# Kernel tuning notes

Hardware: AMD Instinct MI355X
Metric: run time of the kernel (lower is better)

Reference implementation:

```python
import jax, jax.numpy as jnp
import numpy as np

V, J, NB = 6890, 52, 16
NPOSE = (J - 1) * 9  # 459 pose-blendshape features
# Standard SMPL-H kinematic tree: 22 body joints + left hand (wrist 20) + right hand (wrist 21)
PARENTS = np.array([
    -1, 0, 0, 0, 1, 2, 3, 4, 5, 6, 7, 8, 9, 9, 9, 12, 13, 14, 16, 17, 18, 19,
    20, 22, 23, 20, 25, 26, 20, 28, 29, 20, 31, 32, 20, 34, 35,
    21, 37, 38, 21, 40, 41, 21, 43, 44, 21, 46, 47, 21, 49, 50
], dtype=np.int32)


def rot6d_to_matrix(d6):
    # d6: (..., 6) -> (..., 3, 3), rows are the Gram-Schmidt basis (pytorch3d convention)
    a1, a2 = d6[..., :3], d6[..., 3:]
    b1 = a1 / jnp.linalg.norm(a1, axis=-1, keepdims=True)
    a2p = a2 - jnp.sum(b1 * a2, axis=-1, keepdims=True) * b1
    b2 = a2p / jnp.linalg.norm(a2p, axis=-1, keepdims=True)
    b3 = jnp.cross(b1, b2)
    return jnp.stack([b1, b2, b3], axis=-2)


def rigid_transform(rot_mats, joints):
    # rot_mats: (B, J, 3, 3); joints: (B, J, 3) -> relative transforms (B, J, 4, 4)
    rel = jnp.concatenate(
        [joints[..., :1, :], joints[..., 1:, :] - joints[..., PARENTS[1:], :]], axis=-2)
    tm = jnp.concatenate([rot_mats, rel[..., None]], axis=-1)  # (B, J, 3, 4)
    bottom = jnp.zeros(tm.shape[:-2] + (1, 4), dtype=tm.dtype).at[..., 0, 3].set(1.0)
    tm = jnp.concatenate([tm, bottom], axis=-2)  # (B, J, 4, 4)
    chain = [tm[..., 0, :, :]]
    for i in range(1, J):  # fixed 52-joint tree, unrolled
        chain.append(chain[int(PARENTS[i])] @ tm[..., i, :, :])
    transforms = jnp.stack(chain, axis=-3)  # (B, J, 4, 4)
    t_corr = jnp.einsum('bjcd,bjd->bjc', transforms[..., :3, :3], joints)
    return transforms.at[..., :3, 3].add(-t_corr)


def lbs_forward(body_pose, betas, global_orient, transl,
                v_template, shapedirs, posedirs, J_template, J_shapedirs, lbs_weights):
    full_pose = jnp.concatenate([global_orient, body_pose], axis=-2)  # (B, 52, 6)
    rot_mats = rot6d_to_matrix(full_pose)                              # (B, 52, 3, 3)
    joints = J_template + jnp.einsum('bk,jck->bjc', betas, J_shapedirs)
    A = rigid_transform(rot_mats, joints)                              # (B, 52, 4, 4)
    eye = jnp.eye(3, dtype=rot_mats.dtype)
    pose_feature = (rot_mats[..., 1:, :, :] - eye).reshape(rot_mats.shape[0], NPOSE)
    v_posed = (v_template
               + jnp.einsum('bk,vck->bvc', betas, shapedirs)
               + jnp.einsum('bk,kvc->bvc', pose_feature, posedirs))    # (B, V, 3)
    T = jnp.einsum('vj,bjcd->bvcd', lbs_weights, A)                    # (B, V, 4, 4)
    verts = jnp.einsum('bvcd,bvd->bvc', T[..., :3, :3], v_posed) + T[..., :3, 3]
    return verts + transl[..., None, :]


def setup_inputs() -> dict:
    key = jax.random.key(0)
    ks = jax.random.split(key, 10)
    B = 1024
    return {
        'body_pose': jax.random.normal(ks[0], (B, J - 1, 6), jnp.float32),
        'betas': jax.random.normal(ks[1], (B, NB), jnp.float32),
        'global_orient': jax.random.normal(ks[2], (B, 1, 6), jnp.float32),
        'transl': jax.random.normal(ks[3], (B, 3), jnp.float32),
        'v_template': jax.random.normal(ks[4], (V, 3), jnp.float32) * 0.3,
        'shapedirs': jax.random.normal(ks[5], (V, 3, NB), jnp.float32) * 0.01,
        'posedirs': jax.random.normal(ks[6], (NPOSE, V, 3), jnp.float32) * 0.01,
        'J_template': jax.random.normal(ks[7], (J, 3), jnp.float32) * 0.3,
        'J_shapedirs': jax.random.normal(ks[8], (J, 3, NB), jnp.float32) * 0.01,
        'lbs_weights': jax.nn.softmax(jax.random.normal(ks[9], (V, J), jnp.float32) * 2.0, axis=-1),
    }


def reference(body_pose, betas, global_orient, transl,
              v_template, shapedirs, posedirs, J_template, J_shapedirs, lbs_weights):
    return lbs_forward(body_pose, betas, global_orient, transl,
                       v_template, shapedirs, posedirs, J_template, J_shapedirs, lbs_weights)
```

## Files before the change

kernel.cpp:

```cpp
#include <hip/hip_runtime.h>

typedef unsigned short u16;
typedef __bf16  bf16x8 __attribute__((ext_vector_type(8)));
typedef float   f32x4  __attribute__((ext_vector_type(4)));
typedef unsigned int u32x4 __attribute__((ext_vector_type(4)));

#define B_SZ   1024
#define V_SZ   6890
#define VPADB  6912
#define J_SZ   52
#define NB_SZ  16
#define NPOSE  459
#define N3     20670
#define NPAD   20736
#define KG     480
#define KA     160
#define MROWS  12288

__constant__ int PARENTS_D[52] = {-1,0,0,0,1,2,3,4,5,6,7,8,9,9,9,12,13,14,16,17,18,19,20,22,23,
                                  20,25,26,20,28,29,20,31,32,20,34,35,21,37,38,21,40,41,21,43,44,
                                  21,46,47,21,49,50};

__device__ __forceinline__ u16 f2b(float f) {
  union { float f; unsigned u; } v; v.f = f;
  unsigned r = (v.u + 0x7FFFu + ((v.u >> 16) & 1u)) >> 16;
  return (u16)r;
}
__device__ __forceinline__ float b2f(u16 h) {
  union { unsigned u; float f; } v; v.u = ((unsigned)h) << 16;
  return v.f;
}
__device__ __forceinline__ void async16(const void* g, void* l) {
  __builtin_amdgcn_global_load_lds((const __attribute__((address_space(1))) void*)g,
                                   (__attribute__((address_space(3))) void*)l, 16, 0, 0);
}

__global__ __launch_bounds__(256) void k0_build_pdt(const float* __restrict__ posedirs,
                                                    const float* __restrict__ shapedirs,
                                                    u16* __restrict__ PDt)
{
  __shared__ u16 tile[32][33];
  const int tx = threadIdx.x;
  const int ty = threadIdx.y;
  const int n0 = blockIdx.x * 32;
  const int k0 = blockIdx.y * 32;
#pragma unroll
  for (int i = 0; i < 4; ++i) {
    int k = k0 + ty + i*8;
    int n = n0 + tx;
    float val = 0.f;
    if (n < N3) {
      if (k < NPOSE)              val = posedirs[(size_t)k * N3 + n];
      else if (k < NPOSE + NB_SZ) val = shapedirs[(size_t)n * NB_SZ + (k - NPOSE)];
    }
    tile[ty + i*8][tx] = f2b(val);
  }
  __syncthreads();
#pragma unroll
  for (int i = 0; i < 4; ++i) {
    int n = n0 + ty + i*8;
    int k = k0 + tx;
    PDt[(size_t)n * KG + k] = tile[tx][ty + i*8];
  }
}

__global__ __launch_bounds__(256) void k0w_build_wb(const float* __restrict__ lbsw,
                                                    u16* __restrict__ WB)
{
  __shared__ __align__(16) u16 wtile[64 * KA];
  const int tid = threadIdx.x;
  const int v0  = blockIdx.x * 64;
  const int vl  = tid >> 2;
  const int v   = v0 + vl;
  const int jseg = (tid & 3) * 13;

  wtile[(tid >> 2) * KA + 156 + (tid & 3)] = 0;

#pragma unroll
  for (int jj = 0; jj < 13; ++jj) {
    int j = jseg + jj;
    float wv = (v < V_SZ) ? lbsw[(size_t)v * J_SZ + j] : 0.f;
    u16 hi = f2b(wv);
    u16 lo = f2b(wv - b2f(hi));
    wtile[vl * KA + j]        = hi;
    wtile[vl * KA + 52 + j]   = hi;
    wtile[vl * KA + 104 + j]  = lo;
  }
  __syncthreads();
  u32x4*       dst = (u32x4*)(WB + (size_t)v0 * KA);
  const u32x4* src = (const u32x4*)wtile;
  for (int i = tid; i < 64 * KA / 8; i += 256) dst[i] = src[i];
}

__global__ __launch_bounds__(64) void k1_prep(const float* __restrict__ body_pose,
                                              const float* __restrict__ betas,
                                              const float* __restrict__ global_orient,
                                              const float* __restrict__ J_template,
                                              const float* __restrict__ J_shapedirs,
                                              u16* __restrict__ AH,
                                              u16* __restrict__ PF)
{
  __shared__ float R[J_SZ][9];
  __shared__ float jts[J_SZ][3];
  __shared__ float G[J_SZ][12];
  __shared__ u16   AHs[12 * KA];
  const int b   = blockIdx.x;
  const int tid = threadIdx.x;

  for (int i = tid; i < 12 * KA / 2; i += 64) ((unsigned*)AHs)[i] = 0u;

  if (tid < J_SZ) {
    const float* d6 = (tid == 0) ? &global_orient[(size_t)b * 6]
                                 : &body_pose[((size_t)b * 51 + (tid - 1)) * 6];
    float a1x = d6[0], a1y = d6[1], a1z = d6[2];
    float a2x = d6[3], a2y = d6[4], a2z = d6[5];
    float inv1 = rsqrtf(a1x*a1x + a1y*a1y + a1z*a1z);
    float b1x = a1x*inv1, b1y = a1y*inv1, b1z = a1z*inv1;
    float d   = b1x*a2x + b1y*a2y + b1z*a2z;
    float ux = a2x - d*b1x, uy = a2y - d*b1y, uz = a2z - d*b1z;
    float inv2 = rsqrtf(ux*ux + uy*uy + uz*uz);
    float b2x = ux*inv2, b2y = uy*inv2, b2z = uz*inv2;
    float b3x = b1y*b2z - b1z*b2y;
    float b3y = b1z*b2x - b1x*b2z;
    float b3z = b1x*b2y - b1y*b2x;
    R[tid][0]=b1x; R[tid][1]=b1y; R[tid][2]=b1z;
    R[tid][3]=b2x; R[tid][4]=b2y; R[tid][5]=b2z;
    R[tid][6]=b3x; R[tid][7]=b3y; R[tid][8]=b3z;
#pragma unroll
    for (int c = 0; c < 3; ++c) {
      float s = J_template[tid*3 + c];
#pragma unroll
      for (int k = 0; k < NB_SZ; ++k)
        s += betas[(size_t)b*NB_SZ + k] * J_shapedirs[(tid*3 + c)*NB_SZ + k];
      jts[tid][c] = s;
    }
  }
  __syncthreads();

  if (tid == 0) {
#pragma unroll
    for (int c = 0; c < 3; ++c) {
      G[0][c*4+0] = R[0][c*3+0];
      G[0][c*4+1] = R[0][c*3+1];
      G[0][c*4+2] = R[0][c*3+2];
      G[0][c*4+3] = jts[0][c];
    }
    for (int j = 1; j < J_SZ; ++j) {
      int p = PARENTS_D[j];
      float r0 = jts[j][0] - jts[p][0];
      float r1 = jts[j][1] - jts[p][1];
      float r2 = jts[j][2] - jts[p][2];
      for (int c = 0; c < 3; ++c) {
        float g0 = G[p][c*4+0], g1 = G[p][c*4+1], g2 = G[p][c*4+2];
        G[j][c*4+0] = g0*R[j][0] + g1*R[j][3] + g2*R[j][6];
        G[j][c*4+1] = g0*R[j][1] + g1*R[j][4] + g2*R[j][7];
        G[j][c*4+2] = g0*R[j][2] + g1*R[j][5] + g2*R[j][8];
        G[j][c*4+3] = g0*r0 + g1*r1 + g2*r2 + G[p][c*4+3];
      }
    }
  }
  __syncthreads();

  if (tid < J_SZ) {
    float o[12];
#pragma unroll
    for (int i = 0; i < 12; ++i) o[i] = G[tid][i];
#pragma unroll
    for (int c = 0; c < 3; ++c)
      o[c*4+3] -= o[c*4+0]*jts[tid][0] + o[c*4+1]*jts[tid][1] + o[c*4+2]*jts[tid][2];
#pragma unroll
    for (int cd = 0; cd < 12; ++cd) {
      u16 hi = f2b(o[cd]);
      u16 lo = f2b(o[cd] - b2f(hi));
      AHs[cd*KA + tid]        = hi;
      AHs[cd*KA + 52 + tid]   = lo;
      AHs[cd*KA + 104 + tid]  = hi;
    }
  }

  for (int k = tid; k < KG; k += 64) {
    float val = 0.f;
    if (k < NPOSE) {
      int j  = k / 9 + 1;
      int rc = k - (j - 1) * 9;
      val = R[j][rc] - ((rc == 0 || rc == 4 || rc == 8) ? 1.f : 0.f);
    } else if (k < NPOSE + NB_SZ) {
      val = betas[(size_t)b*NB_SZ + (k - NPOSE)];
    }
    PF[(size_t)b*KG + k] = f2b(val);
  }

  __syncthreads();
  unsigned* dst = (unsigned*)(AH + (size_t)b * 12 * KA);
  for (int i = tid; i < 12 * KA / 2; i += 64) dst[i] = ((const unsigned*)AHs)[i];
}

__global__ __launch_bounds__(256) void k2_gemm(const u16* __restrict__ PF,
                                               const u16* __restrict__ PDt,
                                               const float* __restrict__ vtmpl,
                                               u16* __restrict__ VP)
{
  __shared__ __align__(16) u16 lA[128*32];
  __shared__ __align__(16) u16 lB[128*32];
  const int tid  = threadIdx.x;
  const int lane = tid & 63;
  const int w    = tid >> 6;
  const int n0   = blockIdx.x * 128;
  const int b0   = blockIdx.y * 128;
  const int moff = (w & 1) * 64;
  const int noff = (w >> 1) * 64;
  const int q    = lane >> 4;
  const int lrow = lane & 15;

  f32x4 acc[4][4];
#pragma unroll
  for (int i = 0; i < 4; ++i)
#pragma unroll
    for (int j = 0; j < 4; ++j) { f32x4 z = {0.f,0.f,0.f,0.f}; acc[i][j] = z; }

  int aoff[4], boff[4];
#pragma unroll
  for (int i = 0; i < 4; ++i) {
    int ra = moff + i*16 + lrow;
    aoff[i] = ra*32 + (q ^ ((ra + (ra >> 2)) & 3)) * 8;
    int rb = noff + i*16 + lrow;
    boff[i] = rb*32 + (q ^ ((rb + (rb >> 2)) & 3)) * 8;
  }
  int srow[2], schunk[2];
#pragma unroll
  for (int t = 0; t < 2; ++t) {
    int i = (t*4 + w)*64 + lane;
    int r = i >> 2;
    srow[t]   = r;
    schunk[t] = (i & 3) ^ ((r + (r >> 2)) & 3);
  }

  for (int k0 = 0; k0 < KG; k0 += 32) {
#pragma unroll
    for (int t = 0; t < 2; ++t) {
      async16(PF  + (size_t)(b0 + srow[t])*KG + k0 + schunk[t]*8, &lA[(t*4 + w)*512]);
      async16(PDt + (size_t)(n0 + srow[t])*KG + k0 + schunk[t]*8, &lB[(t*4 + w)*512]);
    }
    __syncthreads();
    bf16x8 af[4], bfv[4];
#pragma unroll
    for (int i = 0; i < 4; ++i) af[i]  = *(const bf16x8*)&lA[aoff[i]];
#pragma unroll
    for (int i = 0; i < 4; ++i) bfv[i] = *(const bf16x8*)&lB[boff[i]];
#pragma unroll
    for (int i = 0; i < 4; ++i)
#pragma unroll
      for (int j = 0; j < 4; ++j)
        acc[i][j] = __builtin_amdgcn_mfma_f32_16x16x32_bf16(af[i], bfv[j], acc[i][j], 0, 0, 0);
    __syncthreads();
  }

#pragma unroll
  for (int i = 0; i < 4; ++i) {
    int brow = b0 + moff + i*16 + q*4;
#pragma unroll
    for (int j = 0; j < 4; ++j) {
      int n = n0 + noff + j*16 + lrow;
      if (n < N3) {
        float bias = vtmpl[n];
#pragma unroll
        for (int r = 0; r < 4; ++r)
          VP[(size_t)(brow + r)*NPAD + n] = f2b(acc[i][j][r] + bias);
      }
    }
  }
}

__global__ __launch_bounds__(256) void k4_blend(const u16* __restrict__ AH,
                                                const u16* __restrict__ WB,
                                                const u16* __restrict__ VP,
                                                const float* __restrict__ transl,
                                                float* __restrict__ out)
{
  __shared__ __align__(16) u16 lA[2][4096];
  __shared__ __align__(16) u16 lB[2][4096];
  const int tid  = threadIdx.x;
  const int lane = tid & 63;
  const int w    = tid >> 6;
  const int n0   = blockIdx.x * 128;
  const int m0   = blockIdx.y * 128;
  const int moff = (w & 1) * 64;
  const int noff = (w >> 1) * 64;
  const int q    = lane >> 4;
  const int lrow = lane & 15;

  int srow[2], schunk[2];
#pragma unroll
  for (int t = 0; t < 2; ++t) {
    int i = (t*4 + w)*64 + lane;
    int r = i >> 2;
    srow[t]   = r;
    schunk[t] = (i & 3) ^ ((r + (r >> 2)) & 3);
  }

#define K4_STAGE(buf, seg)                                                          \
  {                                                                                 \
    const int kk = (seg) * 32;                                                      \
    _Pragma("unroll")                                                               \
    for (int t = 0; t < 2; ++t) {                                                   \
      async16(AH + (size_t)(m0 + srow[t])*KA + kk + schunk[t]*8,                    \
              &lA[buf][(t*4 + w)*512]);                                             \
      async16(WB + (size_t)(n0 + srow[t])*KA + kk + schunk[t]*8,                    \
              &lB[buf][(t*4 + w)*512]);                                             \
    }                                                                               \
  }

  K4_STAGE(0, 0);

  int   bp[4], cp[4];
  float tr[4];
#pragma unroll
  for (int i = 0; i < 4; ++i) {
    int gq = (m0 + moff + i*16) / 4 + q;
    bp[i] = gq / 3;
    cp[i] = gq - bp[i]*3;
    tr[i] = transl[bp[i]*3 + cp[i]];
  }
  u16 pv[4][4][3];
#pragma unroll
  for (int i = 0; i < 4; ++i) {
    const u16* vpb = VP + (size_t)bp[i] * NPAD;
#pragma unroll
    for (int j = 0; j < 4; ++j) {
      const int v = n0 + noff + j*16 + lrow;
      pv[i][j][0] = vpb[(size_t)v*3 + 0];
      pv[i][j][1] = vpb[(size_t)v*3 + 1];
      pv[i][j][2] = vpb[(size_t)v*3 + 2];
    }
  }

  f32x4 acc[4][4];
#pragma unroll
  for (int i = 0; i < 4; ++i)
#pragma unroll
    for (int j = 0; j < 4; ++j) { f32x4 z = {0.f,0.f,0.f,0.f}; acc[i][j] = z; }

  int aoff[4], boff[4];
#pragma unroll
  for (int i = 0; i < 4; ++i) {
    int ra = moff + i*16 + lrow;
    aoff[i] = ra*32 + (q ^ ((ra + (ra >> 2)) & 3)) * 8;
    int rb = noff + i*16 + lrow;
    boff[i] = rb*32 + (q ^ ((rb + (rb >> 2)) & 3)) * 8;
  }

  __syncthreads();

#pragma unroll
  for (int seg = 0; seg < 5; ++seg) {
    const int cur = seg & 1;
    if (seg < 4) K4_STAGE(cur ^ 1, seg + 1);
    bf16x8 af[4], bfv[4];
#pragma unroll
    for (int i = 0; i < 4; ++i) af[i]  = *(const bf16x8*)&lA[cur][aoff[i]];
#pragma unroll
    for (int i = 0; i < 4; ++i) bfv[i] = *(const bf16x8*)&lB[cur][boff[i]];
#pragma unroll
    for (int i = 0; i < 4; ++i)
#pragma unroll
      for (int j = 0; j < 4; ++j)
        acc[i][j] = __builtin_amdgcn_mfma_f32_16x16x32_bf16(af[i], bfv[j], acc[i][j], 0, 0, 0);
    if (seg < 4) __syncthreads();
  }
#undef K4_STAGE

#pragma unroll
  for (int i = 0; i < 4; ++i) {
    float* ob = out + (size_t)bp[i] * (V_SZ * 3);
#pragma unroll
    for (int j = 0; j < 4; ++j) {
      const int v = n0 + noff + j*16 + lrow;
      if (v < V_SZ) {
        float p0 = b2f(pv[i][j][0]);
        float p1 = b2f(pv[i][j][1]);
        float p2 = b2f(pv[i][j][2]);
        f32x4 a = acc[i][j];
        ob[(size_t)v*3 + cp[i]] = a[0]*p0 + a[1]*p1 + a[2]*p2 + a[3] + tr[i];
      }
    }
  }
}

extern "C" void kernel_launch(void* const* d_in, const int* in_sizes, int n_in,
                              void* d_out, int out_size, void* d_ws, size_t ws_size,
                              hipStream_t stream) {
  const float* body_pose     = (const float*)d_in[0];
  const float* betas         = (const float*)d_in[1];
  const float* global_orient = (const float*)d_in[2];
  const float* transl        = (const float*)d_in[3];
  const float* v_template    = (const float*)d_in[4];
  const float* shapedirs     = (const float*)d_in[5];
  const float* posedirs      = (const float*)d_in[6];
  const float* J_template    = (const float*)d_in[7];
  const float* J_shapedirs   = (const float*)d_in[8];
  const float* lbsw          = (const float*)d_in[9];
  float* out = (float*)d_out;

  char* ws = (char*)d_ws;
  u16* PF  = (u16*)(ws);
  u16* AH  = (u16*)(ws + 1048576u);
  u16* WB  = (u16*)(ws + 6291456u);
  u16* PDt = (u16*)(ws + 8503296u);
  u16* VP  = (u16*)(ws + 28409856u);

  k0_build_pdt<<<dim3(648, 15), dim3(32, 8), 0, stream>>>(posedirs, shapedirs, PDt);
  k0w_build_wb<<<dim3(VPADB / 64), dim3(256), 0, stream>>>(lbsw, WB);
  k1_prep<<<dim3(1024), dim3(64), 0, stream>>>(body_pose, betas, global_orient,
                                               J_template, J_shapedirs, AH, PF);
  k2_gemm<<<dim3(162, 8), dim3(256), 0, stream>>>(PF, PDt, v_template, VP);
  k4_blend<<<dim3(VPADB / 128, MROWS / 128), dim3(256), 0, stream>>>(AH, WB, VP, transl, out);
}
```

Measured before the change: 280.2 us.

## Merge prep kernels into one launch and double-buffer GEMM LDS loads

Result: faster. 269.1 us (-4.0%).

```diff
diff --git a/kernel.cpp b/kernel.cpp
--- a/kernel.cpp
+++ b/kernel.cpp
@@ -17,6 +17,10 @@
 #define KA     160
 #define MROWS  12288
 
+#define NK1    (B_SZ / 4)
+#define NK0W   (VPADB / 64)
+#define NK0    (648 * 15)
+
 __constant__ int PARENTS_D[52] = {-1,0,0,0,1,2,3,4,5,6,7,8,9,9,9,12,13,14,16,17,18,19,20,22,23,
                                   20,25,26,20,28,29,20,31,32,20,34,35,21,37,38,21,40,41,21,43,44,
                                   21,46,47,21,49,50};
@@ -35,122 +39,74 @@
                                    (__attribute__((address_space(3))) void*)l, 16, 0, 0);
 }
 
-__global__ __launch_bounds__(256) void k0_build_pdt(const float* __restrict__ posedirs,
-                                                    const float* __restrict__ shapedirs,
-                                                    u16* __restrict__ PDt)
-{
-  __shared__ u16 tile[32][33];
-  const int tx = threadIdx.x;
-  const int ty = threadIdx.y;
-  const int n0 = blockIdx.x * 32;
-  const int k0 = blockIdx.y * 32;
-#pragma unroll
-  for (int i = 0; i < 4; ++i) {
-    int k = k0 + ty + i*8;
-    int n = n0 + tx;
-    float val = 0.f;
-    if (n < N3) {
-      if (k < NPOSE)              val = posedirs[(size_t)k * N3 + n];
-      else if (k < NPOSE + NB_SZ) val = shapedirs[(size_t)n * NB_SZ + (k - NPOSE)];
-    }
-    tile[ty + i*8][tx] = f2b(val);
-  }
-  __syncthreads();
-#pragma unroll
-  for (int i = 0; i < 4; ++i) {
-    int n = n0 + ty + i*8;
-    int k = k0 + tx;
-    PDt[(size_t)n * KG + k] = tile[tx][ty + i*8];
-  }
-}
-
-__global__ __launch_bounds__(256) void k0w_build_wb(const float* __restrict__ lbsw,
-                                                    u16* __restrict__ WB)
-{
-  __shared__ __align__(16) u16 wtile[64 * KA];
-  const int tid = threadIdx.x;
-  const int v0  = blockIdx.x * 64;
-  const int vl  = tid >> 2;
-  const int v   = v0 + vl;
-  const int jseg = (tid & 3) * 13;
-
-  wtile[(tid >> 2) * KA + 156 + (tid & 3)] = 0;
-
-#pragma unroll
-  for (int jj = 0; jj < 13; ++jj) {
-    int j = jseg + jj;
-    float wv = (v < V_SZ) ? lbsw[(size_t)v * J_SZ + j] : 0.f;
-    u16 hi = f2b(wv);
-    u16 lo = f2b(wv - b2f(hi));
-    wtile[vl * KA + j]        = hi;
-    wtile[vl * KA + 52 + j]   = hi;
-    wtile[vl * KA + 104 + j]  = lo;
-  }
-  __syncthreads();
-  u32x4*       dst = (u32x4*)(WB + (size_t)v0 * KA);
-  const u32x4* src = (const u32x4*)wtile;
-  for (int i = tid; i < 64 * KA / 8; i += 256) dst[i] = src[i];
-}
-
-__global__ __launch_bounds__(64) void k1_prep(const float* __restrict__ body_pose,
+__global__ __launch_bounds__(256) void k_prep(const float* __restrict__ posedirs,
+                                              const float* __restrict__ shapedirs,
+                                              const float* __restrict__ lbsw,
+                                              const float* __restrict__ body_pose,
                                               const float* __restrict__ betas,
                                               const float* __restrict__ global_orient,
                                               const float* __restrict__ J_template,
                                               const float* __restrict__ J_shapedirs,
+                                              u16* __restrict__ PDt,
+                                              u16* __restrict__ WB,
                                               u16* __restrict__ AH,
                                               u16* __restrict__ PF)
 {
-  __shared__ float R[J_SZ][9];
-  __shared__ float jts[J_SZ][3];
-  __shared__ float G[J_SZ][12];
-  __shared__ u16   AHs[12 * KA];
-  const int b   = blockIdx.x;
+  __shared__ __align__(16) char smem[35328];
+  const int bid = blockIdx.x;
   const int tid = threadIdx.x;
 
-  for (int i = tid; i < 12 * KA / 2; i += 64) ((unsigned*)AHs)[i] = 0u;
-
-  if (tid < J_SZ) {
-    const float* d6 = (tid == 0) ? &global_orient[(size_t)b * 6]
-                                 : &body_pose[((size_t)b * 51 + (tid - 1)) * 6];
-    float a1x = d6[0], a1y = d6[1], a1z = d6[2];
-    float a2x = d6[3], a2y = d6[4], a2z = d6[5];
-    float inv1 = rsqrtf(a1x*a1x + a1y*a1y + a1z*a1z);
-    float b1x = a1x*inv1, b1y = a1y*inv1, b1z = a1z*inv1;
-    float d   = b1x*a2x + b1y*a2y + b1z*a2z;
-    float ux = a2x - d*b1x, uy = a2y - d*b1y, uz = a2z - d*b1z;
-    float inv2 = rsqrtf(ux*ux + uy*uy + uz*uz);
-    float b2x = ux*inv2, b2y = uy*inv2, b2z = uz*inv2;
-    float b3x = b1y*b2z - b1z*b2y;
-    float b3y = b1z*b2x - b1x*b2z;
-    float b3z = b1x*b2y - b1y*b2x;
-    R[tid][0]=b1x; R[tid][1]=b1y; R[tid][2]=b1z;
-    R[tid][3]=b2x; R[tid][4]=b2y; R[tid][5]=b2z;
-    R[tid][6]=b3x; R[tid][7]=b3y; R[tid][8]=b3z;
-#pragma unroll
-    for (int c = 0; c < 3; ++c) {
-      float s = J_template[tid*3 + c];
-#pragma unroll
-      for (int k = 0; k < NB_SZ; ++k)
-        s += betas[(size_t)b*NB_SZ + k] * J_shapedirs[(tid*3 + c)*NB_SZ + k];
-      jts[tid][c] = s;
-    }
-  }
-  __syncthreads();
-
-  if (tid == 0) {
-#pragma unroll
-    for (int c = 0; c < 3; ++c) {
+  if (bid < NK1) {
+    const int g = tid >> 6;
+    const int t = tid & 63;
+    const int b = bid * 4 + g;
+    char* base = smem + g * 8832;
+    float (*R)[9]   = (float(*)[9])(base);
+    float (*jts)[3] = (float(*)[3])(base + 1872);
+    float (*G)[12]  = (float(*)[12])(base + 2496);
+    u16*   AHs      = (u16*)(base + 4992);
+
+    for (int i = t; i < 12 * KA / 2; i += 64) ((unsigned*)AHs)[i] = 0u;
+
+    if (t < J_SZ) {
+      const float* d6 = (t == 0) ? &global_orient[(size_t)b * 6]
+                                 : &body_pose[((size_t)b * 51 + (t - 1)) * 6];
+      float a1x = d6[0], a1y = d6[1], a1z = d6[2];
+      float a2x = d6[3], a2y = d6[4], a2z = d6[5];
+      float inv1 = rsqrtf(a1x*a1x + a1y*a1y + a1z*a1z);
+      float b1x = a1x*inv1, b1y = a1y*inv1, b1z = a1z*inv1;
+      float d   = b1x*a2x + b1y*a2y + b1z*a2z;
+      float ux = a2x - d*b1x, uy = a2y - d*b1y, uz = a2z - d*b1z;
+      float inv2 = rsqrtf(ux*ux + uy*uy + uz*uz);
+      float b2x = ux*inv2, b2y = uy*inv2, b2z = uz*inv2;
+      float b3x = b1y*b2z - b1z*b2y;
+      float b3y = b1z*b2x - b1x*b2z;
+      float b3z = b1x*b2y - b1y*b2x;
+      R[t][0]=b1x; R[t][1]=b1y; R[t][2]=b1z;
+      R[t][3]=b2x; R[t][4]=b2y; R[t][5]=b2z;
+      R[t][6]=b3x; R[t][7]=b3y; R[t][8]=b3z;
+#pragma unroll
+      for (int c = 0; c < 3; ++c) {
+        float s = J_template[t*3 + c];
+#pragma unroll
+        for (int k = 0; k < NB_SZ; ++k)
+          s += betas[(size_t)b*NB_SZ + k] * J_shapedirs[(t*3 + c)*NB_SZ + k];
+        jts[t][c] = s;
+      }
+    }
+    __syncthreads();
+
+    if (t < 3) {
+      const int c = t;
       G[0][c*4+0] = R[0][c*3+0];
       G[0][c*4+1] = R[0][c*3+1];
       G[0][c*4+2] = R[0][c*3+2];
       G[0][c*4+3] = jts[0][c];
-    }
-    for (int j = 1; j < J_SZ; ++j) {
-      int p = PARENTS_D[j];
-      float r0 = jts[j][0] - jts[p][0];
-      float r1 = jts[j][1] - jts[p][1];
-      float r2 = jts[j][2] - jts[p][2];
-      for (int c = 0; c < 3; ++c) {
+      for (int j = 1; j < J_SZ; ++j) {
+        int p = PARENTS_D[j];
+        float r0 = jts[j][0] - jts[p][0];
+        float r1 = jts[j][1] - jts[p][1];
+        float r2 = jts[j][2] - jts[p][2];
         float g0 = G[p][c*4+0], g1 = G[p][c*4+1], g2 = G[p][c*4+2];
         G[j][c*4+0] = g0*R[j][0] + g1*R[j][3] + g2*R[j][6];
         G[j][c*4+1] = g0*R[j][1] + g1*R[j][4] + g2*R[j][7];
@@ -158,41 +114,91 @@
         G[j][c*4+3] = g0*r0 + g1*r1 + g2*r2 + G[p][c*4+3];
       }
     }
-  }
-  __syncthreads();
-
-  if (tid < J_SZ) {
-    float o[12];
-#pragma unroll
-    for (int i = 0; i < 12; ++i) o[i] = G[tid][i];
-#pragma unroll
-    for (int c = 0; c < 3; ++c)
-      o[c*4+3] -= o[c*4+0]*jts[tid][0] + o[c*4+1]*jts[tid][1] + o[c*4+2]*jts[tid][2];
-#pragma unroll
-    for (int cd = 0; cd < 12; ++cd) {
-      u16 hi = f2b(o[cd]);
-      u16 lo = f2b(o[cd] - b2f(hi));
-      AHs[cd*KA + tid]        = hi;
-      AHs[cd*KA + 52 + tid]   = lo;
-      AHs[cd*KA + 104 + tid]  = hi;
-    }
-  }
-
-  for (int k = tid; k < KG; k += 64) {
-    float val = 0.f;
-    if (k < NPOSE) {
-      int j  = k / 9 + 1;
-      int rc = k - (j - 1) * 9;
-      val = R[j][rc] - ((rc == 0 || rc == 4 || rc == 8) ? 1.f : 0.f);
-    } else if (k < NPOSE + NB_SZ) {
-      val = betas[(size_t)b*NB_SZ + (k - NPOSE)];
-    }
-    PF[(size_t)b*KG + k] = f2b(val);
-  }
-
-  __syncthreads();
-  unsigned* dst = (unsigned*)(AH + (size_t)b * 12 * KA);
-  for (int i = tid; i < 12 * KA / 2; i += 64) dst[i] = ((const unsigned*)AHs)[i];
+    __syncthreads();
+
+    if (t < J_SZ) {
+      float o[12];
+#pragma unroll
+      for (int i = 0; i < 12; ++i) o[i] = G[t][i];
+#pragma unroll
+      for (int c = 0; c < 3; ++c)
+        o[c*4+3] -= o[c*4+0]*jts[t][0] + o[c*4+1]*jts[t][1] + o[c*4+2]*jts[t][2];
+#pragma unroll
+      for (int cd = 0; cd < 12; ++cd) {
+        u16 hi = f2b(o[cd]);
+        u16 lo = f2b(o[cd] - b2f(hi));
+        AHs[cd*KA + t]        = hi;
+        AHs[cd*KA + 52 + t]   = lo;
+        AHs[cd*KA + 104 + t]  = hi;
+      }
+    }
+
+    for (int k = t; k < KG; k += 64) {
+      float val = 0.f;
+      if (k < NPOSE) {
+        int j  = k / 9 + 1;
+        int rc = k - (j - 1) * 9;
+        val = R[j][rc] - ((rc == 0 || rc == 4 || rc == 8) ? 1.f : 0.f);
+      } else if (k < NPOSE + NB_SZ) {
+        val = betas[(size_t)b*NB_SZ + (k - NPOSE)];
+      }
+      PF[(size_t)b*KG + k] = f2b(val);
+    }
+
+    __syncthreads();
+    unsigned* dst = (unsigned*)(AH + (size_t)b * 12 * KA);
+    for (int i = t; i < 12 * KA / 2; i += 64) dst[i] = ((const unsigned*)AHs)[i];
+
+  } else if (bid < NK1 + NK0W) {
+    u16* wtile = (u16*)smem;
+    const int v0  = (bid - NK1) * 64;
+    const int vl  = tid >> 2;
+    const int v   = v0 + vl;
+    const int jseg = (tid & 3) * 13;
+
+    wtile[vl * KA + 156 + (tid & 3)] = 0;
+
+#pragma unroll
+    for (int jj = 0; jj < 13; ++jj) {
+      int j = jseg + jj;
+      float wv = (v < V_SZ) ? lbsw[(size_t)v * J_SZ + j] : 0.f;
+      u16 hi = f2b(wv);
+      u16 lo = f2b(wv - b2f(hi));
+      wtile[vl * KA + j]        = hi;
+      wtile[vl * KA + 52 + j]   = hi;
+      wtile[vl * KA + 104 + j]  = lo;
+    }
+    __syncthreads();
+    u32x4*       dst = (u32x4*)(WB + (size_t)v0 * KA);
+    const u32x4* src = (const u32x4*)wtile;
+    for (int i = tid; i < 64 * KA / 8; i += 256) dst[i] = src[i];
+
+  } else {
+    u16 (*tile)[33] = (u16(*)[33])smem;
+    const int cb = bid - NK1 - NK0W;
+    const int tx = tid & 31;
+    const int ty = tid >> 5;
+    const int n0 = (cb % 648) * 32;
+    const int k0 = (cb / 648) * 32;
+#pragma unroll
+    for (int i = 0; i < 4; ++i) {
+      int k = k0 + ty + i*8;
+      int n = n0 + tx;
+      float val = 0.f;
+      if (n < N3) {
+        if (k < NPOSE)              val = posedirs[(size_t)k * N3 + n];
+        else if (k < NPOSE + NB_SZ) val = shapedirs[(size_t)n * NB_SZ + (k - NPOSE)];
+      }
+      tile[ty + i*8][tx] = f2b(val);
+    }
+    __syncthreads();
+#pragma unroll
+    for (int i = 0; i < 4; ++i) {
+      int n = n0 + ty + i*8;
+      int k = k0 + tx;
+      PDt[(size_t)n * KG + k] = tile[tx][ty + i*8];
+    }
+  }
 }
 
 __global__ __launch_bounds__(256) void k2_gemm(const u16* __restrict__ PF,
@@ -200,8 +206,8 @@
                                                const float* __restrict__ vtmpl,
                                                u16* __restrict__ VP)
 {
-  __shared__ __align__(16) u16 lA[128*32];
-  __shared__ __align__(16) u16 lB[128*32];
+  __shared__ __align__(16) u16 lA[2][4096];
+  __shared__ __align__(16) u16 lB[2][4096];
   const int tid  = threadIdx.x;
   const int lane = tid & 63;
   const int w    = tid >> 6;
@@ -235,25 +241,37 @@
     schunk[t] = (i & 3) ^ ((r + (r >> 2)) & 3);
   }
 
-  for (int k0 = 0; k0 < KG; k0 += 32) {
-#pragma unroll
-    for (int t = 0; t < 2; ++t) {
-      async16(PF  + (size_t)(b0 + srow[t])*KG + k0 + schunk[t]*8, &lA[(t*4 + w)*512]);
-      async16(PDt + (size_t)(n0 + srow[t])*KG + k0 + schunk[t]*8, &lB[(t*4 + w)*512]);
-    }
-    __syncthreads();
+#define K2_STAGE(buf, seg)                                                          \
+  {                                                                                 \
+    const int kk = (seg) * 32;                                                      \
+    _Pragma("unroll")                                                               \
+    for (int t = 0; t < 2; ++t) {                                                   \
+      async16(PF  + (size_t)(b0 + srow[t])*KG + kk + schunk[t]*8,                   \
+              &lA[buf][(t*4 + w)*512]);                                             \
+      async16(PDt + (size_t)(n0 + srow[t])*KG + kk + schunk[t]*8,                   \
+              &lB[buf][(t*4 + w)*512]);                                             \
+    }                                                                               \
+  }
+
+  K2_STAGE(0, 0);
+  __syncthreads();
+
+  for (int seg = 0; seg < 15; ++seg) {
+    const int cur = seg & 1;
+    if (seg < 14) K2_STAGE(cur ^ 1, seg + 1);
     bf16x8 af[4], bfv[4];
 #pragma unroll
-    for (int i = 0; i < 4; ++i) af[i]  = *(const bf16x8*)&lA[aoff[i]];
-#pragma unroll
-    for (int i = 0; i < 4; ++i) bfv[i] = *(const bf16x8*)&lB[boff[i]];
+    for (int i = 0; i < 4; ++i) af[i]  = *(const bf16x8*)&lA[cur][aoff[i]];
+#pragma unroll
+    for (int i = 0; i < 4; ++i) bfv[i] = *(const bf16x8*)&lB[cur][boff[i]];
 #pragma unroll
     for (int i = 0; i < 4; ++i)
 #pragma unroll
       for (int j = 0; j < 4; ++j)
         acc[i][j] = __builtin_amdgcn_mfma_f32_16x16x32_bf16(af[i], bfv[j], acc[i][j], 0, 0, 0);
-    __syncthreads();
-  }
+    if (seg < 14) __syncthreads();
+  }
+#undef K2_STAGE
 
 #pragma unroll
   for (int i = 0; i < 4; ++i) {
@@ -408,10 +426,9 @@
   u16* PDt = (u16*)(ws + 8503296u);
   u16* VP  = (u16*)(ws + 28409856u);
 
-  k0_build_pdt<<<dim3(648, 15), dim3(32, 8), 0, stream>>>(posedirs, shapedirs, PDt);
-  k0w_build_wb<<<dim3(VPADB / 64), dim3(256), 0, stream>>>(lbsw, WB);
-  k1_prep<<<dim3(1024), dim3(64), 0, stream>>>(body_pose, betas, global_orient,
-                                               J_template, J_shapedirs, AH, PF);
+  k_prep<<<dim3(NK1 + NK0W + NK0), dim3(256), 0, stream>>>(
+      posedirs, shapedirs, lbsw, body_pose, betas, global_orient,
+      J_template, J_shapedirs, PDt, WB, AH, PF);
   k2_gemm<<<dim3(162, 8), dim3(256), 0, stream>>>(PF, PDt, v_template, VP);
   k4_blend<<<dim3(VPADB / 128, MROWS / 128), dim3(256), 0, stream>>>(AH, WB, VP, transl, out);
 }
```
